# Optimization experiments

Measured on AMD Instinct MI355X. Metric: run time of the kernel, lower is better.

## Reference

```python
import jax, jax.numpy as jnp
import numpy as np


def setup_inputs() -> dict:
    key = jax.random.key(0)
    k1, k2, k3, k4 = jax.random.split(key, 4)
    B, D_vis, E, N = 512, 4096, 1024, 512
    vf = jax.random.normal(k1, (B, D_vis), dtype=jnp.float32)
    p_lfs = jax.random.normal(k2, (B, E), dtype=jnp.float32)
    n_lfs = jax.random.normal(k3, (N, E), dtype=jnp.float32)
    W = jax.random.normal(k4, (E, D_vis), dtype=jnp.float32) * (1.0 / np.sqrt(D_vis))
    b = jnp.zeros((E,), dtype=jnp.float32)
    return {"vf": vf, "p_lfs": p_lfs, "n_lfs": n_lfs, "W": W, "b": b}


def _partial_order_sim(hypers, hypos):
    # -||relu(hypers - hypos)||_2 along last dim
    act = jax.nn.relu(hypers - hypos)
    return -jnp.sqrt(jnp.sum(act * act, axis=-1))


def reference(vf, p_lfs, n_lfs, W, b):
    # vf: [B, D_vis], W: [E, D_vis] -> vf_emb: [B, E]
    vf_emb = jnp.einsum("bd,ed->be", vf, W) + b
    # positive scores: [B]
    p_scores = _partial_order_sim(p_lfs, vf_emb)
    # negative scores, batched over B: n_lfs [N,E] vs vf_emb [B,E] -> [B,N]
    n_scores = _partial_order_sim(n_lfs[None, :, :], vf_emb[:, None, :])
    # score_stack: [B, 1+N]
    return jnp.concatenate([p_scores[:, None], n_scores], axis=1)
```

## Files before the change

### kernel.cpp

```cpp
#include <hip/hip_runtime.h>
#include <hip/hip_bf16.h>

constexpr int B = 512;
constexpr int D = 4096;
constexpr int E = 1024;
constexpr int N = 512;
constexpr int KSW = 16;
constexpr int KSG = 4;
constexpr int KC = D / KSW;
constexpr int NSTEP = KC / 32;
constexpr int ES = 8;
constexpr int EC = E / ES;
constexpr int DEPTH = 2;

typedef __attribute__((ext_vector_type(8))) short bf16x8;
typedef __attribute__((ext_vector_type(4))) float f32x4;
typedef _Float16 h2 __attribute__((ext_vector_type(2)));
typedef _Float16 h4 __attribute__((ext_vector_type(4)));
typedef _Float16 h8 __attribute__((ext_vector_type(8)));

typedef __attribute__((address_space(3))) void lds_void;
typedef const __attribute__((address_space(1))) void gbl_void;

__device__ __forceinline__ unsigned short f2bf(float f) {
    __hip_bfloat16 h = __float2bfloat16(f);
    return *reinterpret_cast<unsigned short*>(&h);
}

#if __has_builtin(__builtin_amdgcn_fdot2)
__device__ __forceinline__ float fdot2(h2 a, h2 b, float c) {
    return __builtin_amdgcn_fdot2(a, b, c, false);
}
#else
__device__ __forceinline__ float fdot2(h2 a, h2 b, float c) {
    return c + (float)a[0] * (float)b[0] + (float)a[1] * (float)b[1];
}
#endif

__global__ __launch_bounds__(256) void cvt_all(
    const float* __restrict__ vf, const float* __restrict__ W,
    const float* __restrict__ n_lfs,
    unsigned short* __restrict__ vfB, unsigned short* __restrict__ WB,
    _Float16* __restrict__ n16)
{
    const int bid = blockIdx.x;
    if (bid < 3072) {
        const float* src;
        unsigned short* dst;
        int i;
        if (bid < 1024) { src = vf; dst = vfB; i = (bid * 256 + threadIdx.x) * 8; }
        else           { src = W;  dst = WB;  i = ((bid - 1024) * 256 + threadIdx.x) * 8; }
        float4 v0 = *(const float4*)(src + i);
        float4 v1 = *(const float4*)(src + i + 4);
        bf16x8 o;
        o[0] = (short)f2bf(v0.x); o[1] = (short)f2bf(v0.y);
        o[2] = (short)f2bf(v0.z); o[3] = (short)f2bf(v0.w);
        o[4] = (short)f2bf(v1.x); o[5] = (short)f2bf(v1.y);
        o[6] = (short)f2bf(v1.z); o[7] = (short)f2bf(v1.w);
        *(bf16x8*)(dst + i) = o;
    } else {
        const int i = ((bid - 3072) * 256 + threadIdx.x) * 8;
        float4 v0 = *(const float4*)(n_lfs + i);
        float4 v1 = *(const float4*)(n_lfs + i + 4);
        h8 o;
        o[0] = (_Float16)v0.x; o[1] = (_Float16)v0.y;
        o[2] = (_Float16)v0.z; o[3] = (_Float16)v0.w;
        o[4] = (_Float16)v1.x; o[5] = (_Float16)v1.y;
        o[6] = (_Float16)v1.z; o[7] = (_Float16)v1.w;
        *(h8*)(n16 + i) = o;
    }
}

__global__ __launch_bounds__(256) void gemm_lds(
    const unsigned short* __restrict__ vf,
    const unsigned short* __restrict__ W,
    _Float16* __restrict__ part)
{
    __shared__ __align__(16) char smem[70656];

    const int t = threadIdx.x;
    const int w = t >> 6;
    const int L = t & 63;

    const int id = blockIdx.x + 16 * blockIdx.y + 128 * blockIdx.z;
    const int l  = (id & 7) * 64 + (id >> 3);
    const int z  = l >> 7;
    const int n0 = (l & 15) * 64;
    const int m0 = ((l >> 4) & 7) * 64;

    char* stg = smem + w * 16384;

    const int subrow = L >> 2;
    const int qstg = (L & 3) ^ ((L >> 2) & 3) ^ ((L >> 4) & 3);
    const int kbeg = (z * 4 + w) * KC;
    const unsigned short* aSrc[4];
    const unsigned short* bSrc[4];
    #pragma unroll
    for (int c = 0; c < 4; ++c) {
        aSrc[c] = vf + (size_t)(m0 + c * 16 + subrow) * D + kbeg + qstg * 8;
        bSrc[c] = W  + (size_t)(n0 + c * 16 + subrow) * D + kbeg + qstg * 8;
    }

    const int r16 = L & 15;
    const int quad = L >> 4;
    const int swz = quad ^ (r16 & 3) ^ ((r16 >> 2) & 3);
    const int aoff = r16 * 64 + swz * 16;

    f32x4 acc[4][4] = {};

    auto issue = [&](int step, int buf) {
        const size_t koff = (size_t)step * 32;
        #pragma unroll
        for (int c = 0; c < 4; ++c) {
            __builtin_amdgcn_global_load_lds(
                (gbl_void*)(aSrc[c] + koff),
                (lds_void*)(stg + buf * 4096 + c * 1024), 16, 0, 0);
            __builtin_amdgcn_global_load_lds(
                (gbl_void*)(bSrc[c] + koff),
                (lds_void*)(stg + 8192 + buf * 4096 + c * 1024), 16, 0, 0);
        }
    };

    issue(0, 0);
    issue(1, 1);

    #define GSTEP(S, WC, ISS)                                                  \
    {                                                                          \
        const int buf_ = (S) & 1;                                              \
        __builtin_amdgcn_s_waitcnt(WC);                                        \
        bf16x8 af[4], bg[4];                                                   \
        _Pragma("unroll")                                                      \
        for (int i = 0; i < 4; ++i)                                            \
            af[i] = *(const bf16x8*)(stg + buf_ * 4096 + i * 1024 + aoff);     \
        _Pragma("unroll")                                                      \
        for (int j = 0; j < 4; ++j)                                            \
            bg[j] = *(const bf16x8*)(stg + 8192 + buf_ * 4096 + j * 1024 + aoff); \
        __builtin_amdgcn_s_setprio(1);                                         \
        _Pragma("unroll")                                                      \
        for (int i = 0; i < 4; ++i)                                            \
            _Pragma("unroll")                                                  \
            for (int j = 0; j < 4; ++j)                                        \
                acc[i][j] = __builtin_amdgcn_mfma_f32_16x16x32_bf16(           \
                    af[i], bg[j], acc[i][j], 0, 0, 0);                         \
        __builtin_amdgcn_s_setprio(0);                                         \
        if (ISS) issue((S) + DEPTH, buf_);                                     \
    }

    #pragma unroll 1
    for (int s = 0; s < NSTEP - 1; ++s)
        GSTEP(s, 0x0F78, s + DEPTH < NSTEP);
    GSTEP(NSTEP - 1, 0x0F70, false);
    #undef GSTEP

    __syncthreads();
    float* ctw = (float*)smem + w * 4416;
    #pragma unroll
    for (int i = 0; i < 4; ++i)
        #pragma unroll
        for (int j = 0; j < 4; ++j)
            #pragma unroll
            for (int r = 0; r < 4; ++r)
                ctw[(i * 16 + quad * 4 + r) * 69 + (j * 16 + r16)] = acc[i][j][r];
    __syncthreads();

    const int row = t >> 2;
    const int cb  = (t & 3) * 16;
    const float* p0 = (const float*)smem + row * 69 + cb;
    float s[16];
    #pragma unroll
    for (int u = 0; u < 16; ++u)
        s[u] = (p0[u] + p0[4416 + u]) + (p0[8832 + u] + p0[13248 + u]);
    _Float16* po = part + (size_t)z * B * E + (size_t)(m0 + row) * E + n0 + cb;
    h8 v0, v1;
    #pragma unroll
    for (int u = 0; u < 8; ++u) { v0[u] = (_Float16)s[u]; v1[u] = (_Float16)s[u + 8]; }
    *(h8*)po = v0;
    *(h8*)(po + 8) = v1;
}

__global__ __launch_bounds__(256) void reduce_emb(
    const _Float16* __restrict__ part, const float* __restrict__ bias,
    const float* __restrict__ p_lfs,
    _Float16* __restrict__ emb16, float* __restrict__ out)
{
    const int b = blockIdx.x;
    const int e = threadIdx.x * 4;
    const size_t base = (size_t)b * E + e;
    float4 s = *(const float4*)(bias + e);
    #pragma unroll
    for (int ks = 0; ks < KSG; ++ks) {
        h4 p = *(const h4*)(part + (size_t)ks * B * E + base);
        s.x += (float)p[0]; s.y += (float)p[1];
        s.z += (float)p[2]; s.w += (float)p[3];
    }
    h4 o;
    o[0] = (_Float16)s.x; o[1] = (_Float16)s.y;
    o[2] = (_Float16)s.z; o[3] = (_Float16)s.w;
    *(h4*)(emb16 + base) = o;

    const float4 pl = *(const float4*)(p_lfs + base);
    float d, a = 0.f;
    d = pl.x - s.x; d = fmaxf(d, 0.f); a = fmaf(d, d, a);
    d = pl.y - s.y; d = fmaxf(d, 0.f); a = fmaf(d, d, a);
    d = pl.z - s.z; d = fmaxf(d, 0.f); a = fmaf(d, d, a);
    d = pl.w - s.w; d = fmaxf(d, 0.f); a = fmaf(d, d, a);
    #pragma unroll
    for (int off = 32; off; off >>= 1) a += __shfl_down(a, off, 64);
    __shared__ float red[4];
    if ((threadIdx.x & 63) == 0) red[threadIdx.x >> 6] = a;
    __syncthreads();
    if (threadIdx.x == 0)
        out[(size_t)b * 513] = -sqrtf(red[0] + red[1] + red[2] + red[3]);
}

__global__ __launch_bounds__(256, 4) void scores_part(
    const _Float16* __restrict__ emb16,
    const _Float16* __restrict__ n16,
    _Float16* __restrict__ pn)
{
    constexpr int LDH = EC + 8;
    __shared__ _Float16 eS[64 * LDH];
    __shared__ _Float16 nS[64 * LDH];

    const int t  = threadIdx.x;
    const int n0 = blockIdx.x * 64;
    const int b0 = blockIdx.y * 64;
    const int e0 = blockIdx.z * EC;

    {
        const int row = t >> 2;
        const int cb  = (t & 3) * 32;
        const _Float16* ep = emb16 + (size_t)(b0 + row) * E + e0 + cb;
        const _Float16* np = n16   + (size_t)(n0 + row) * E + e0 + cb;
        _Float16* ed = &eS[row * LDH + cb];
        _Float16* nd = &nS[row * LDH + cb];
        #pragma unroll
        for (int q = 0; q < 4; ++q) {
            h8 v = *(const h8*)(ep + q * 8);
            h8 w = *(const h8*)(np + q * 8);
            *(h8*)(ed + q * 8) = -v;
            *(h8*)(nd + q * 8) = w;
        }
    }
    __syncthreads();

    const int ty = t >> 4;
    const int tx = t & 15;

    float acc[4][4] = {};
    const h8 z8 = {};

    #pragma unroll 2
    for (int e = 0; e < EC; e += 8) {
        h8 a[4], c[4];
        #pragma unroll
        for (int r = 0; r < 4; ++r)
            a[r] = *(const h8*)&eS[(ty + 16 * r) * LDH + e];
        #pragma unroll
        for (int q = 0; q < 4; ++q)
            c[q] = *(const h8*)&nS[(tx + 16 * q) * LDH + e];
        #pragma unroll
        for (int r = 0; r < 4; ++r)
            #pragma unroll
            for (int q = 0; q < 4; ++q) {
                h8 d = c[q] + a[r];
                d = __builtin_elementwise_max(d, z8);
                h2 d0 = __builtin_shufflevector(d, d, 0, 1);
                h2 d1 = __builtin_shufflevector(d, d, 2, 3);
                h2 d2 = __builtin_shufflevector(d, d, 4, 5);
                h2 d3 = __builtin_shufflevector(d, d, 6, 7);
                acc[r][q] = fdot2(d0, d0, acc[r][q]);
                acc[r][q] = fdot2(d1, d1, acc[r][q]);
                acc[r][q] = fdot2(d2, d2, acc[r][q]);
                acc[r][q] = fdot2(d3, d3, acc[r][q]);
            }
    }

    _Float16* po = pn + (size_t)blockIdx.z * B * N;
    #pragma unroll
    for (int r = 0; r < 4; ++r) {
        const size_t ob = (size_t)(b0 + ty + 16 * r) * N;
        #pragma unroll
        for (int q = 0; q < 4; ++q)
            po[ob + n0 + tx + 16 * q] = (_Float16)acc[r][q];
    }
}

__global__ __launch_bounds__(256) void scores_final(
    const _Float16* __restrict__ pn,
    float* __restrict__ out)
{
    const int i = blockIdx.x * 256 + threadIdx.x;
    const int b = i >> 9;
    const int n = i & (N - 1);
    float s = 0.f;
    #pragma unroll
    for (int z = 0; z < ES; ++z)
        s += (float)pn[(size_t)z * B * N + i];
    out[(size_t)b * 513 + 1 + n] = -sqrtf(s);
}

extern "C" void kernel_launch(void* const* d_in, const int* in_sizes, int n_in,
                              void* d_out, int out_size, void* d_ws, size_t ws_size,
                              hipStream_t stream) {
    const float* vf    = (const float*)d_in[0];
    const float* p_lfs = (const float*)d_in[1];
    const float* n_lfs = (const float*)d_in[2];
    const float* W     = (const float*)d_in[3];
    const float* bias  = (const float*)d_in[4];
    float* out = (float*)d_out;

    char* ws = (char*)d_ws;
    _Float16*       pg    = (_Float16*)ws;
    _Float16*       pn    = (_Float16*)(ws + ((size_t)4 << 20));
    unsigned short* vfB   = (unsigned short*)(ws + ((size_t)8 << 20));
    unsigned short* WB    = (unsigned short*)(ws + ((size_t)12 << 20));
    _Float16*       emb16 = (_Float16*)(ws + ((size_t)20 << 20));
    _Float16*       n16   = (_Float16*)(ws + ((size_t)21 << 20));

    cvt_all<<<3328, 256, 0, stream>>>(vf, W, n_lfs, vfB, WB, n16);

    dim3 g1(E / 64, B / 64, KSG);
    gemm_lds<<<g1, 256, 0, stream>>>(vfB, WB, pg);

    reduce_emb<<<B, 256, 0, stream>>>(pg, bias, p_lfs, emb16, out);

    dim3 g3(N / 64, B / 64, ES);
    scores_part<<<g3, 256, 0, stream>>>(emb16, n16, pn);

    scores_final<<<(B * N) / 256, 256, 0, stream>>>(pn, out);
}
```

Measured before the change: 112.9 us.

## Fuse split-K reduction and positive scores into GEMM via last-block atomic counter

Measured after the change: 196.4 us. +74.0%, slower.

```diff
diff --git a/kernel.cpp b/kernel.cpp
--- a/kernel.cpp
+++ b/kernel.cpp
@@ -5,9 +5,8 @@
 constexpr int D = 4096;
 constexpr int E = 1024;
 constexpr int N = 512;
-constexpr int KSW = 16;
 constexpr int KSG = 4;
-constexpr int KC = D / KSW;
+constexpr int KC = 256;
 constexpr int NSTEP = KC / 32;
 constexpr int ES = 8;
 constexpr int EC = E / ES;
@@ -41,9 +40,16 @@
     const float* __restrict__ vf, const float* __restrict__ W,
     const float* __restrict__ n_lfs,
     unsigned short* __restrict__ vfB, unsigned short* __restrict__ WB,
-    _Float16* __restrict__ n16)
+    _Float16* __restrict__ n16,
+    float* __restrict__ psum, unsigned int* __restrict__ cnt)
 {
     const int bid = blockIdx.x;
+    if (bid == 3328) {
+        const int t = threadIdx.x;
+        if (t < 128) ((f32x4*)psum)[t] = (f32x4){0.f, 0.f, 0.f, 0.f};
+        else if (t < 160) ((uint4*)cnt)[t - 128] = (uint4){0u, 0u, 0u, 0u};
+        return;
+    }
     if (bid < 3072) {
         const float* src;
         unsigned short* dst;
@@ -71,12 +77,18 @@
     }
 }
 
-__global__ __launch_bounds__(256) void gemm_lds(
+__global__ __launch_bounds__(256) void gemm_fused(
     const unsigned short* __restrict__ vf,
     const unsigned short* __restrict__ W,
-    _Float16* __restrict__ part)
+    const float* __restrict__ bias,
+    const float* __restrict__ p_lfs,
+    _Float16* __restrict__ part,
+    _Float16* __restrict__ emb16,
+    float* __restrict__ psum,
+    unsigned int* __restrict__ cnt)
 {
     __shared__ __align__(16) char smem[70656];
+    __shared__ int lastFlag;
 
     const int t = threadIdx.x;
     const int w = t >> 6;
@@ -87,6 +99,7 @@
     const int z  = l >> 7;
     const int n0 = (l & 15) * 64;
     const int m0 = ((l >> 4) & 7) * 64;
+    const int tileId = ((l >> 4) & 7) * 16 + (l & 15);
 
     char* stg = smem + w * 16384;
 
@@ -170,47 +183,57 @@
     #pragma unroll
     for (int u = 0; u < 16; ++u)
         s[u] = (p0[u] + p0[4416 + u]) + (p0[8832 + u] + p0[13248 + u]);
+
     _Float16* po = part + (size_t)z * B * E + (size_t)(m0 + row) * E + n0 + cb;
     h8 v0, v1;
     #pragma unroll
     for (int u = 0; u < 8; ++u) { v0[u] = (_Float16)s[u]; v1[u] = (_Float16)s[u + 8]; }
     *(h8*)po = v0;
     *(h8*)(po + 8) = v1;
-}
-
-__global__ __launch_bounds__(256) void reduce_emb(
-    const _Float16* __restrict__ part, const float* __restrict__ bias,
-    const float* __restrict__ p_lfs,
-    _Float16* __restrict__ emb16, float* __restrict__ out)
-{
-    const int b = blockIdx.x;
-    const int e = threadIdx.x * 4;
-    const size_t base = (size_t)b * E + e;
-    float4 s = *(const float4*)(bias + e);
-    #pragma unroll
-    for (int ks = 0; ks < KSG; ++ks) {
-        h4 p = *(const h4*)(part + (size_t)ks * B * E + base);
-        s.x += (float)p[0]; s.y += (float)p[1];
-        s.z += (float)p[2]; s.w += (float)p[3];
-    }
-    h4 o;
-    o[0] = (_Float16)s.x; o[1] = (_Float16)s.y;
-    o[2] = (_Float16)s.z; o[3] = (_Float16)s.w;
-    *(h4*)(emb16 + base) = o;
-
-    const float4 pl = *(const float4*)(p_lfs + base);
-    float d, a = 0.f;
-    d = pl.x - s.x; d = fmaxf(d, 0.f); a = fmaf(d, d, a);
-    d = pl.y - s.y; d = fmaxf(d, 0.f); a = fmaf(d, d, a);
-    d = pl.z - s.z; d = fmaxf(d, 0.f); a = fmaf(d, d, a);
-    d = pl.w - s.w; d = fmaxf(d, 0.f); a = fmaf(d, d, a);
-    #pragma unroll
-    for (int off = 32; off; off >>= 1) a += __shfl_down(a, off, 64);
-    __shared__ float red[4];
-    if ((threadIdx.x & 63) == 0) red[threadIdx.x >> 6] = a;
-    __syncthreads();
-    if (threadIdx.x == 0)
-        out[(size_t)b * 513] = -sqrtf(red[0] + red[1] + red[2] + red[3]);
+
+    __threadfence();
+    __syncthreads();
+    if (t == 0)
+        lastFlag = (atomicAdd(&cnt[tileId], 1u) == 3u);
+    __syncthreads();
+    if (!lastFlag) return;
+    __threadfence();
+
+    #pragma unroll
+    for (int zz = 0; zz < KSG; ++zz) {
+        if (zz == z) continue;
+        const _Float16* ps = part + (size_t)zz * B * E + (size_t)(m0 + row) * E + n0 + cb;
+        h8 u0 = *(const h8*)ps;
+        h8 u1 = *(const h8*)(ps + 8);
+        #pragma unroll
+        for (int u = 0; u < 8; ++u) { s[u] += (float)u0[u]; s[u + 8] += (float)u1[u]; }
+    }
+    #pragma unroll
+    for (int q = 0; q < 4; ++q) {
+        const float4 bl = *(const float4*)(bias + n0 + cb + q * 4);
+        s[q * 4]     += bl.x; s[q * 4 + 1] += bl.y;
+        s[q * 4 + 2] += bl.z; s[q * 4 + 3] += bl.w;
+    }
+
+    const size_t obase = (size_t)(m0 + row) * E + n0 + cb;
+    #pragma unroll
+    for (int u = 0; u < 8; ++u) { v0[u] = (_Float16)s[u]; v1[u] = (_Float16)s[u + 8]; }
+    *(h8*)(emb16 + obase) = v0;
+    *(h8*)(emb16 + obase + 8) = v1;
+
+    float a = 0.f;
+    #pragma unroll
+    for (int q = 0; q < 4; ++q) {
+        const float4 pl = *(const float4*)(p_lfs + obase + q * 4);
+        float d;
+        d = pl.x - s[q * 4];     d = fmaxf(d, 0.f); a = fmaf(d, d, a);
+        d = pl.y - s[q * 4 + 1]; d = fmaxf(d, 0.f); a = fmaf(d, d, a);
+        d = pl.z - s[q * 4 + 2]; d = fmaxf(d, 0.f); a = fmaf(d, d, a);
+        d = pl.w - s[q * 4 + 3]; d = fmaxf(d, 0.f); a = fmaf(d, d, a);
+    }
+    a += __shfl_down(a, 2, 4);
+    a += __shfl_down(a, 1, 4);
+    if ((t & 3) == 0) atomicAdd(psum + m0 + row, a);
 }
 
 __global__ __launch_bounds__(256, 4) void scores_part(
@@ -288,8 +311,14 @@
 
 __global__ __launch_bounds__(256) void scores_final(
     const _Float16* __restrict__ pn,
+    const float* __restrict__ psum,
     float* __restrict__ out)
 {
+    if (blockIdx.x >= 1024) {
+        const int idx = (blockIdx.x - 1024) * 256 + threadIdx.x;
+        out[(size_t)idx * 513] = -sqrtf(psum[idx]);
+        return;
+    }
     const int i = blockIdx.x * 256 + threadIdx.x;
     const int b = i >> 9;
     const int n = i & (N - 1);
@@ -317,16 +346,16 @@
     unsigned short* WB    = (unsigned short*)(ws + ((size_t)12 << 20));
     _Float16*       emb16 = (_Float16*)(ws + ((size_t)20 << 20));
     _Float16*       n16   = (_Float16*)(ws + ((size_t)21 << 20));
-
-    cvt_all<<<3328, 256, 0, stream>>>(vf, W, n_lfs, vfB, WB, n16);
+    float*          psum  = (float*)(ws + ((size_t)22 << 20));
+    unsigned int*   cnt   = (unsigned int*)(ws + ((size_t)22 << 20) + 4096);
+
+    cvt_all<<<3329, 256, 0, stream>>>(vf, W, n_lfs, vfB, WB, n16, psum, cnt);
 
     dim3 g1(E / 64, B / 64, KSG);
-    gemm_lds<<<g1, 256, 0, stream>>>(vfB, WB, pg);
-
-    reduce_emb<<<B, 256, 0, stream>>>(pg, bias, p_lfs, emb16, out);
+    gemm_fused<<<g1, 256, 0, stream>>>(vfB, WB, bias, p_lfs, pg, emb16, psum, cnt);
 
     dim3 g3(N / 64, B / 64, ES);
     scores_part<<<g3, 256, 0, stream>>>(emb16, n16, pn);
 
-    scores_final<<<(B * N) / 256, 256, 0, stream>>>(pn, out);
-}
+    scores_final<<<1026, 256, 0, stream>>>(pn, psum, out);
+}
```
